# Performance work log

Hardware: AMD Instinct MI355X
Metric: run time of the kernel (lower is better)

## Reference

```python
import jax, jax.numpy as jnp
import numpy as np

K = 8
DIM = 64
NUM_BLOCKS = 12
BN_EPS = 1e-5
LRELU_SLOPE = 0.01  # torch nn.LeakyReLU default negative_slope


def knn_indices(xyz, k):
    # xyz: [b, 3, n] -> idx [b, n, k] of k nearest neighbors (self included)
    x = jnp.transpose(xyz, (0, 2, 1))  # [b, n, 3]
    sq = jnp.sum(x * x, axis=-1)  # [b, n]
    d2 = sq[:, :, None] - 2.0 * jnp.einsum('bnd,bmd->bnm', x, x) + sq[:, None, :]
    _, idx = jax.lax.top_k(-d2, k)  # k smallest distances
    return idx


def group_point(points, idx):
    # points [b, d, n], idx [b, n, k] -> grouped [b, d, k, n]
    g = jax.vmap(lambda p, i: p[:, i])(points, idx)  # [b, d, n, k]
    return jnp.transpose(g, (0, 1, 3, 2))


def setup_inputs() -> dict:
    key = jax.random.key(0)
    ks = jax.random.split(key, 6)
    b, n = 8, 4096
    xyz = jax.random.normal(ks[0], (b, 3, n), dtype=jnp.float32)
    points = jax.random.normal(ks[1], (b, DIM, n), dtype=jnp.float32)
    # per-block params (note: the module's second Conv2d per block is never used
    # in forward — layers[4*idx+2] is applied to both center and grouped points)
    conv_w = jax.random.normal(ks[2], (NUM_BLOCKS, DIM, DIM), dtype=jnp.float32) * (1.0 / np.sqrt(DIM))
    conv_b = jax.random.normal(ks[3], (NUM_BLOCKS, DIM), dtype=jnp.float32) * 0.01
    bn_gamma = 1.0 + 0.1 * jax.random.normal(ks[4], (NUM_BLOCKS, DIM), dtype=jnp.float32)
    bn_beta = 0.1 * jax.random.normal(ks[5], (NUM_BLOCKS, DIM), dtype=jnp.float32)
    return {"xyz": xyz, "points": points, "conv_w": conv_w, "conv_b": conv_b,
            "bn_gamma": bn_gamma, "bn_beta": bn_beta}


def reference(xyz, points, conv_w, conv_b, bn_gamma, bn_beta):
    idx = knn_indices(xyz, K)  # fixed graph, computed once in block 0

    def block(p, params):
        w, b, g, be = params  # [DIM,DIM], [DIM], [DIM], [DIM]
        shortcut = p
        # BatchNorm1d (training-mode batch stats over batch & point dims)
        mean = jnp.mean(p, axis=(0, 2), keepdims=True)
        var = jnp.var(p, axis=(0, 2), keepdims=True)
        h = (p - mean) * jax.lax.rsqrt(var + BN_EPS) * g[None, :, None] + be[None, :, None]
        # LeakyReLU
        h = jnp.where(h >= 0, h, LRELU_SLOPE * h)
        # gather neighbor features: [b, d, k, n]
        grouped = group_point(h, idx)
        # shared 1x1 conv on center and grouped points
        center = jnp.einsum('od,bdn->bon', w, h) + b[None, :, None]            # [b,d,n]
        gconv = jnp.einsum('od,bdkn->bokn', w, grouped) + b[None, :, None, None]  # [b,d,k,n]
        # mean over concat([center[:, :, None], gconv], axis=2) == (center + sum_k gconv) / (k+1)
        new_p = (center + jnp.sum(gconv, axis=2)) / (K + 1) + shortcut
        return new_p, None

    out, _ = jax.lax.scan(block, points, (conv_w, conv_b, bn_gamma, bn_beta))
    return out
```

## Files before the change

kernel.cpp:

```cpp
#include <hip/hip_runtime.h>
#include <hip/hip_bf16.h>

#define NB     8
#define NPTS   4096
#define DIMC   64
#define KNN_K  8
#define NBLK   12
#define NREP   8

__global__ void zero_stats_kernel(float* __restrict__ stats) {
    int i = threadIdx.x + blockIdx.x * 256;
    if (i < 13 * NREP * 128) stats[i] = 0.0f;
}

__global__ __launch_bounds__(256) void prep_kernel(
        const float* __restrict__ xyz, float4* __restrict__ pts4g) {
#pragma clang fp contract(off)
    int g = blockIdx.x * 256 + threadIdx.x;
    int b = g >> 12, j = g & 4095;
    const float* xb = xyz + (size_t)b * 3 * NPTS;
    float x = xb[j];
    float y = xb[NPTS + j];
    float z = xb[2 * NPTS + j];
    float sq = (x * x + y * y) + z * z;
    pts4g[g] = make_float4(x, y, z, sq);
}

__global__ __launch_bounds__(256) void cast_kernel(
        const float* __restrict__ pts,
        float* __restrict__ P0, float* __restrict__ stats0) {
    __shared__ __align__(16) float tr[64 * 65];
    __shared__ float slotA[4 * 64], slotB[4 * 64];
    int wg = blockIdx.x;
    int b = wg & 7;
    int n0 = (wg >> 3) << 6;
    int rep = (wg >> 3) & (NREP - 1);
    int tid = threadIdx.x;
    int lane6 = tid & 63;
    int grp = tid >> 6;

    #pragma unroll
    for (int k = 0; k < 16; ++k) {
        int d = grp + (k << 2);
        float v = pts[(((size_t)((b << 6) + d)) << 12) + n0 + lane6];
        tr[d * 65 + lane6] = v;
    }
    __syncthreads();
    int c = lane6;
    float s = 0.0f, s2 = 0.0f;
    #pragma unroll
    for (int k = 0; k < 16; ++k) {
        int p = grp + (k << 2);
        float v = tr[c * 65 + p];
        P0[((size_t)((b << 12) + n0 + p)) * 64 + c] = v;
        s += v; s2 += v * v;
    }
    slotA[grp * 64 + c] = s;
    slotB[grp * 64 + c] = s2;
    __syncthreads();
    if (tid < 64) {
        float t = slotA[tid] + slotA[64 + tid] + slotA[128 + tid] + slotA[192 + tid];
        atomicAdd(&stats0[rep * 128 + tid], t);
    } else if (tid < 128) {
        int cc = tid - 64;
        float t = slotB[cc] + slotB[64 + cc] + slotB[128 + cc] + slotB[192 + cc];
        atomicAdd(&stats0[rep * 128 + 64 + cc], t);
    }
}

__global__ __launch_bounds__(512) void knn_kernel(
        const float4* __restrict__ pts4g, int* __restrict__ idx) {
#pragma clang fp contract(off)
    __shared__ __align__(16) float4 cand[2048];
    __shared__ double stash[4 * 9 * 128];
    int wg = blockIdx.x;
    int b = wg >> 5;
    int q0 = (wg & 31) << 7;
    int tid = threadIdx.x;

    int lane  = tid & 63;
    int wave  = tid >> 6;
    int chunk = wave & 3;
    int qgrp  = wave >> 2;
    int q_l   = (qgrp << 6) | lane;

    const float4* cb = pts4g + ((size_t)b << 12);
    float4 qp = cb[q0 + q_l];

    double k0, k1, k2, k3, k4, k5, k6, k7;
    k0 = k1 = k2 = k3 = k4 = k5 = k6 = k7 = __builtin_inf();
    float bd7f = 3.4e38f;

    for (int half = 0; half < 2; ++half) {
        if (half) __syncthreads();
        #pragma unroll
        for (int k = 0; k < 4; ++k)
            cand[tid + (k << 9)] = cb[(half << 11) + tid + (k << 9)];
        __syncthreads();

        int jl0 = chunk << 9;
        int jg0 = (half << 11) | (chunk << 9);
        for (int jo = 0; jo < 512; jo += 8) {
            float d2v[8];
            #pragma unroll
            for (int u = 0; u < 8; ++u) {
                float4 p = cand[jl0 + jo + u];
                float dot = (qp.x * p.x + qp.y * p.y) + qp.z * p.z;
                d2v[u] = (qp.w - 2.0f * dot) + p.w;
            }
            #pragma unroll
            for (int u = 0; u < 8; ++u) {
                float d2 = d2v[u];
                if (d2 < bd7f) {
                    unsigned long long kb =
                        __double_as_longlong((double)d2) |
                        (unsigned long long)(jg0 + jo + u);
                    double key = __longlong_as_double(kb);
                    double n0 = fmin(k0, key);
                    double n1 = fmin(k1, fmax(k0, key));
                    double n2 = fmin(k2, fmax(k1, key));
                    double n3 = fmin(k3, fmax(k2, key));
                    double n4 = fmin(k4, fmax(k3, key));
                    double n5 = fmin(k5, fmax(k4, key));
                    double n6 = fmin(k6, fmax(k5, key));
                    double n7 = fmin(k7, fmax(k6, key));
                    k0 = n0; k1 = n1; k2 = n2; k3 = n3;
                    k4 = n4; k5 = n5; k6 = n6; k7 = n7;
                    bd7f = (float)k7;
                }
            }
        }
    }

    {
        double* S = &stash[(chunk * 9) * 128 + q_l];
        S[0 * 128] = k0; S[1 * 128] = k1; S[2 * 128] = k2; S[3 * 128] = k3;
        S[4 * 128] = k4; S[5 * 128] = k5; S[6 * 128] = k6; S[7 * 128] = k7;
        S[8 * 128] = __builtin_inf();
    }
    __syncthreads();

    if (tid < 128) {
        int h0 = 0, h1 = 0, h2 = 0, h3 = 0;
        int* op = idx + ((size_t)(b * NPTS + q0 + tid)) * 8;
        #pragma unroll
        for (int t = 0; t < 8; ++t) {
            double b0 = stash[(0 * 9 + h0) * 128 + tid];
            double b1 = stash[(1 * 9 + h1) * 128 + tid];
            double b2 = stash[(2 * 9 + h2) * 128 + tid];
            double b3 = stash[(3 * 9 + h3) * 128 + tid];
            double best = b0; int bc = 0;
            if (b1 < best) { best = b1; bc = 1; }
            if (b2 < best) { best = b2; bc = 2; }
            if (b3 < best) { best = b3; bc = 3; }
            h0 += (bc == 0); h1 += (bc == 1);
            h2 += (bc == 2); h3 += (bc == 3);
            op[t] = (int)(__double_as_longlong(best) & 0xFFFULL);
        }
    }
}

__global__ __launch_bounds__(256) void block_kernel(
        const float* __restrict__ Pin, float* __restrict__ Pout,
        const float* __restrict__ statsIn, float* __restrict__ statsOut,
        const float* __restrict__ Wp, const float* __restrict__ Bp,
        const float* __restrict__ Gp, const float* __restrict__ Betap,
        const int* __restrict__ gidx, float* __restrict__ dout, int last) {
    __shared__ __align__(16) float Wt[64 * 68];
    __shared__ __align__(16) float mt[64 * 68];
    __shared__ __align__(16) float selft[64 * 64];
    __shared__ __align__(16) int   idxl[64 * 8];
    __shared__ __align__(16) float scale_l[64], shift_l[64], bias_l[64];
    __shared__ float slot[4 * 128];

    int wg = blockIdx.x;
    int b = wg & 7;
    int n0 = (wg >> 3) << 6;
    int rep = (wg >> 3) & (NREP - 1);
    int tid = threadIdx.x;

    const float* Pb = Pin + (((size_t)b) << 18);

    if (tid < 128) {
        ((int4*)idxl)[tid] = ((const int4*)(gidx + ((size_t)(b * NPTS + n0)) * 8))[tid];
    }
    #pragma unroll
    for (int k = 0; k < 4; ++k) {
        int lin = tid + (k << 8);
        ((float4*)selft)[lin] = ((const float4*)&Pb[(size_t)n0 << 6])[lin];
    }
    #pragma unroll
    for (int k = 0; k < 16; ++k) {
        int lin = tid + (k << 8);
        int o = lin >> 6, d = lin & 63;
        Wt[d * 68 + o] = Wp[lin];
    }
    if (tid < 64) {
        int c = tid;
        float sum = 0.0f, sumsq = 0.0f;
        #pragma unroll
        for (int r = 0; r < NREP; ++r) {
            sum   += statsIn[r * 128 + c];
            sumsq += statsIn[r * 128 + 64 + c];
        }
        float mean = sum * (1.0f / 32768.0f);
        float var  = sumsq * (1.0f / 32768.0f) - mean * mean;
        float rs   = 1.0f / sqrtf(var + 1e-5f);
        float sc   = Gp[c] * rs;
        scale_l[c] = sc;
        shift_l[c] = Betap[c] - mean * sc;
        bias_l[c]  = Bp[c];
    }
    __syncthreads();

    {
        int cq = tid & 15;
        int pg = tid >> 4;
        int c4 = cq << 2;
        float4 sc4 = *(const float4*)&scale_l[c4];
        float4 sh4 = *(const float4*)&shift_l[c4];
        #pragma unroll
        for (int i = 0; i < 4; ++i) {
            int pt = (pg << 2) + i;
            int4 ja = *(const int4*)&idxl[pt * 8];
            int4 jb = *(const int4*)&idxl[pt * 8 + 4];
            float4 v[9];
            v[0] = *(const float4*)&selft[(pt << 6) + c4];
            v[1] = *(const float4*)&Pb[(((size_t)ja.x) << 6) + c4];
            v[2] = *(const float4*)&Pb[(((size_t)ja.y) << 6) + c4];
            v[3] = *(const float4*)&Pb[(((size_t)ja.z) << 6) + c4];
            v[4] = *(const float4*)&Pb[(((size_t)ja.w) << 6) + c4];
            v[5] = *(const float4*)&Pb[(((size_t)jb.x) << 6) + c4];
            v[6] = *(const float4*)&Pb[(((size_t)jb.y) << 6) + c4];
            v[7] = *(const float4*)&Pb[(((size_t)jb.z) << 6) + c4];
            v[8] = *(const float4*)&Pb[(((size_t)jb.w) << 6) + c4];
            float4 a = make_float4(0.f, 0.f, 0.f, 0.f);
            #pragma unroll
            for (int k = 0; k < 9; ++k) {
                float hx = v[k].x * sc4.x + sh4.x;
                float hy = v[k].y * sc4.y + sh4.y;
                float hz = v[k].z * sc4.z + sh4.z;
                float hw = v[k].w * sc4.w + sh4.w;
                a.x += fmaxf(hx, 0.01f * hx);
                a.y += fmaxf(hy, 0.01f * hy);
                a.z += fmaxf(hz, 0.01f * hz);
                a.w += fmaxf(hw, 0.01f * hw);
            }
            mt[(c4 + 0) * 68 + pt] = a.x * (1.0f / 9.0f);
            mt[(c4 + 1) * 68 + pt] = a.y * (1.0f / 9.0f);
            mt[(c4 + 2) * 68 + pt] = a.z * (1.0f / 9.0f);
            mt[(c4 + 3) * 68 + pt] = a.w * (1.0f / 9.0f);
        }
    }
    __syncthreads();

    int o0 = (tid & 15) << 2;
    int p0 = (tid >> 4) << 2;
    float4 acc[4];
    {
        float4 bias4 = *(const float4*)&bias_l[o0];
        acc[0] = bias4; acc[1] = bias4; acc[2] = bias4; acc[3] = bias4;
    }
    #pragma unroll
    for (int d = 0; d < 64; ++d) {
        float4 wv = *(const float4*)&Wt[d * 68 + o0];
        float4 a  = *(const float4*)&mt[d * 68 + p0];
        acc[0].x += wv.x * a.x; acc[0].y += wv.y * a.x; acc[0].z += wv.z * a.x; acc[0].w += wv.w * a.x;
        acc[1].x += wv.x * a.y; acc[1].y += wv.y * a.y; acc[1].z += wv.z * a.y; acc[1].w += wv.w * a.y;
        acc[2].x += wv.x * a.z; acc[2].y += wv.y * a.z; acc[2].z += wv.z * a.z; acc[2].w += wv.w * a.z;
        acc[3].x += wv.x * a.w; acc[3].y += wv.y * a.w; acc[3].z += wv.z * a.w; acc[3].w += wv.w * a.w;
    }

    #pragma unroll
    for (int j = 0; j < 4; ++j) {
        float4 r = *(const float4*)&selft[((p0 + j) << 6) + o0];
        acc[j].x += r.x; acc[j].y += r.y; acc[j].z += r.z; acc[j].w += r.w;
    }

    if (!last) {
        float* PbOut = Pout + ((((size_t)b) << 12) + n0) * 64;
        #pragma unroll
        for (int j = 0; j < 4; ++j)
            *(float4*)&PbOut[((size_t)(p0 + j)) * 64 + o0] = acc[j];

        float4 s, s2;
        s.x = acc[0].x + acc[1].x + acc[2].x + acc[3].x;
        s.y = acc[0].y + acc[1].y + acc[2].y + acc[3].y;
        s.z = acc[0].z + acc[1].z + acc[2].z + acc[3].z;
        s.w = acc[0].w + acc[1].w + acc[2].w + acc[3].w;
        s2.x = acc[0].x*acc[0].x + acc[1].x*acc[1].x + acc[2].x*acc[2].x + acc[3].x*acc[3].x;
        s2.y = acc[0].y*acc[0].y + acc[1].y*acc[1].y + acc[2].y*acc[2].y + acc[3].y*acc[3].y;
        s2.z = acc[0].z*acc[0].z + acc[1].z*acc[1].z + acc[2].z*acc[2].z + acc[3].z*acc[3].z;
        s2.w = acc[0].w*acc[0].w + acc[1].w*acc[1].w + acc[2].w*acc[2].w + acc[3].w*acc[3].w;
        #pragma unroll
        for (int m = 16; m <= 32; m <<= 1) {
            s.x += __shfl_xor(s.x, m, 64);  s.y += __shfl_xor(s.y, m, 64);
            s.z += __shfl_xor(s.z, m, 64);  s.w += __shfl_xor(s.w, m, 64);
            s2.x += __shfl_xor(s2.x, m, 64); s2.y += __shfl_xor(s2.y, m, 64);
            s2.z += __shfl_xor(s2.z, m, 64); s2.w += __shfl_xor(s2.w, m, 64);
        }
        if ((tid & 63) < 16) {
            int w = tid >> 6;
            slot[w * 128 + o0 + 0] = s.x;  slot[w * 128 + o0 + 1] = s.y;
            slot[w * 128 + o0 + 2] = s.z;  slot[w * 128 + o0 + 3] = s.w;
            slot[w * 128 + 64 + o0 + 0] = s2.x; slot[w * 128 + 64 + o0 + 1] = s2.y;
            slot[w * 128 + 64 + o0 + 2] = s2.z; slot[w * 128 + 64 + o0 + 3] = s2.w;
        }
        __syncthreads();
        if (tid < 128) {
            float t = slot[tid] + slot[128 + tid] + slot[256 + tid] + slot[384 + tid];
            atomicAdd(&statsOut[rep * 128 + tid], t);
        }
    } else {
        __syncthreads();
        float* stage = mt;
        #pragma unroll
        for (int j = 0; j < 4; ++j) {
            stage[(o0 + 0) * 64 + p0 + j] = acc[j].x;
            stage[(o0 + 1) * 64 + p0 + j] = acc[j].y;
            stage[(o0 + 2) * 64 + p0 + j] = acc[j].z;
            stage[(o0 + 3) * 64 + p0 + j] = acc[j].w;
        }
        __syncthreads();
        #pragma unroll
        for (int k = 0; k < 16; ++k) {
            int lin = tid + (k << 8);
            int o = lin >> 6, pt = lin & 63;
            dout[(((size_t)((b << 6) + o)) << 12) + n0 + pt] = stage[lin];
        }
    }
}

extern "C" void kernel_launch(void* const* d_in, const int* in_sizes, int n_in,
                              void* d_out, int out_size, void* d_ws, size_t ws_size,
                              hipStream_t stream) {
    const float* xyz    = (const float*)d_in[0];
    const float* pts    = (const float*)d_in[1];
    const float* conv_w = (const float*)d_in[2];
    const float* conv_b = (const float*)d_in[3];
    const float* gamma  = (const float*)d_in[4];
    const float* beta   = (const float*)d_in[5];
    float* out = (float*)d_out;

    char* ws = (char*)d_ws;
    float*  P0    = (float*)(ws);
    float*  P1    = (float*)(ws + (size_t)8 * 1024 * 1024);
    int*    idx   = (int*)  (ws + (size_t)16 * 1024 * 1024);
    float*  stats = (float*)(ws + (size_t)17 * 1024 * 1024);
    float4* pts4g = (float4*)(ws + (size_t)18 * 1024 * 1024);

    zero_stats_kernel<<<52, 256, 0, stream>>>(stats);
    prep_kernel<<<128, 256, 0, stream>>>(xyz, pts4g);
    cast_kernel<<<512, 256, 0, stream>>>(pts, P0, stats);
    knn_kernel<<<256, 512, 0, stream>>>(pts4g, idx);

    float* Pbuf[2] = {P0, P1};
    for (int t = 0; t < NBLK; ++t) {
        block_kernel<<<512, 256, 0, stream>>>(
            Pbuf[t & 1], Pbuf[(t + 1) & 1],
            stats + (size_t)t * NREP * 128, stats + (size_t)(t + 1) * NREP * 128,
            conv_w + (size_t)t * 4096, conv_b + (size_t)t * 64,
            gamma + (size_t)t * 64, beta + (size_t)t * 64,
            idx, out, (t == NBLK - 1) ? 1 : 0);
    }
}
```

Before: 326.7 us.

## Split kNN candidates across eight waves and widen block kernel to 512 threads

The kNN kernel now gives each workgroup 64 queries and splits the candidate scan into eight 256-point chunks, one per wave. It launches twice as many workgroups and merges eight partial top-8 lists instead of four. The residual block kernel moves to 512 threads, with each thread computing 2 points instead of 4, which raises thread-level parallelism at the cost of register reuse in the matmul. Stats zeroing is folded into the prep kernel to save one launch. Each kNN workgroup now loads all candidate points into shared memory, so there are twice as many shared-memory fills.

```diff
diff --git a/kernel.cpp b/kernel.cpp
--- a/kernel.cpp
+++ b/kernel.cpp
@@ -8,15 +8,12 @@
 #define NBLK   12
 #define NREP   8
 
-__global__ void zero_stats_kernel(float* __restrict__ stats) {
-    int i = threadIdx.x + blockIdx.x * 256;
-    if (i < 13 * NREP * 128) stats[i] = 0.0f;
-}
-
 __global__ __launch_bounds__(256) void prep_kernel(
-        const float* __restrict__ xyz, float4* __restrict__ pts4g) {
+        const float* __restrict__ xyz, float4* __restrict__ pts4g,
+        float* __restrict__ stats) {
 #pragma clang fp contract(off)
     int g = blockIdx.x * 256 + threadIdx.x;
+    if (g < 13 * NREP * 128) stats[g] = 0.0f;
     int b = g >> 12, j = g & 4095;
     const float* xb = xyz + (size_t)b * 3 * NPTS;
     float x = xb[j];
@@ -72,20 +69,17 @@
         const float4* __restrict__ pts4g, int* __restrict__ idx) {
 #pragma clang fp contract(off)
     __shared__ __align__(16) float4 cand[2048];
-    __shared__ double stash[4 * 9 * 128];
+    __shared__ double stash[8 * 9 * 64];
     int wg = blockIdx.x;
-    int b = wg >> 5;
-    int q0 = (wg & 31) << 7;
+    int b = wg >> 6;
+    int q0 = (wg & 63) << 6;
     int tid = threadIdx.x;
 
     int lane  = tid & 63;
-    int wave  = tid >> 6;
-    int chunk = wave & 3;
-    int qgrp  = wave >> 2;
-    int q_l   = (qgrp << 6) | lane;
+    int chunk = tid >> 6;
 
     const float4* cb = pts4g + ((size_t)b << 12);
-    float4 qp = cb[q0 + q_l];
+    float4 qp = cb[q0 + lane];
 
     double k0, k1, k2, k3, k4, k5, k6, k7;
     k0 = k1 = k2 = k3 = k4 = k5 = k6 = k7 = __builtin_inf();
@@ -98,9 +92,9 @@
             cand[tid + (k << 9)] = cb[(half << 11) + tid + (k << 9)];
         __syncthreads();
 
-        int jl0 = chunk << 9;
-        int jg0 = (half << 11) | (chunk << 9);
-        for (int jo = 0; jo < 512; jo += 8) {
+        int jl0 = chunk << 8;
+        int jg0 = (half << 11) | jl0;
+        for (int jo = 0; jo < 256; jo += 8) {
             float d2v[8];
             #pragma unroll
             for (int u = 0; u < 8; ++u) {
@@ -133,34 +127,42 @@
     }
 
     {
-        double* S = &stash[(chunk * 9) * 128 + q_l];
-        S[0 * 128] = k0; S[1 * 128] = k1; S[2 * 128] = k2; S[3 * 128] = k3;
-        S[4 * 128] = k4; S[5 * 128] = k5; S[6 * 128] = k6; S[7 * 128] = k7;
-        S[8 * 128] = __builtin_inf();
-    }
-    __syncthreads();
-
-    if (tid < 128) {
-        int h0 = 0, h1 = 0, h2 = 0, h3 = 0;
+        double* S = &stash[(chunk * 9) * 64 + lane];
+        S[0 * 64] = k0; S[1 * 64] = k1; S[2 * 64] = k2; S[3 * 64] = k3;
+        S[4 * 64] = k4; S[5 * 64] = k5; S[6 * 64] = k6; S[7 * 64] = k7;
+        S[8 * 64] = __builtin_inf();
+    }
+    __syncthreads();
+
+    if (tid < 64) {
+        int h0 = 0, h1 = 0, h2 = 0, h3 = 0, h4 = 0, h5 = 0, h6 = 0, h7 = 0;
         int* op = idx + ((size_t)(b * NPTS + q0 + tid)) * 8;
         #pragma unroll
         for (int t = 0; t < 8; ++t) {
-            double b0 = stash[(0 * 9 + h0) * 128 + tid];
-            double b1 = stash[(1 * 9 + h1) * 128 + tid];
-            double b2 = stash[(2 * 9 + h2) * 128 + tid];
-            double b3 = stash[(3 * 9 + h3) * 128 + tid];
-            double best = b0; int bc = 0;
-            if (b1 < best) { best = b1; bc = 1; }
-            if (b2 < best) { best = b2; bc = 2; }
-            if (b3 < best) { best = b3; bc = 3; }
-            h0 += (bc == 0); h1 += (bc == 1);
-            h2 += (bc == 2); h3 += (bc == 3);
+            double v0 = stash[(0 * 9 + h0) * 64 + tid];
+            double v1 = stash[(1 * 9 + h1) * 64 + tid];
+            double v2 = stash[(2 * 9 + h2) * 64 + tid];
+            double v3 = stash[(3 * 9 + h3) * 64 + tid];
+            double v4 = stash[(4 * 9 + h4) * 64 + tid];
+            double v5 = stash[(5 * 9 + h5) * 64 + tid];
+            double v6 = stash[(6 * 9 + h6) * 64 + tid];
+            double v7 = stash[(7 * 9 + h7) * 64 + tid];
+            double best = v0; int bc = 0;
+            if (v1 < best) { best = v1; bc = 1; }
+            if (v2 < best) { best = v2; bc = 2; }
+            if (v3 < best) { best = v3; bc = 3; }
+            if (v4 < best) { best = v4; bc = 4; }
+            if (v5 < best) { best = v5; bc = 5; }
+            if (v6 < best) { best = v6; bc = 6; }
+            if (v7 < best) { best = v7; bc = 7; }
+            h0 += (bc == 0); h1 += (bc == 1); h2 += (bc == 2); h3 += (bc == 3);
+            h4 += (bc == 4); h5 += (bc == 5); h6 += (bc == 6); h7 += (bc == 7);
             op[t] = (int)(__double_as_longlong(best) & 0xFFFULL);
         }
     }
 }
 
-__global__ __launch_bounds__(256) void block_kernel(
+__global__ __launch_bounds__(512) void block_kernel(
         const float* __restrict__ Pin, float* __restrict__ Pout,
         const float* __restrict__ statsIn, float* __restrict__ statsOut,
         const float* __restrict__ Wp, const float* __restrict__ Bp,
@@ -171,7 +173,7 @@
     __shared__ __align__(16) float selft[64 * 64];
     __shared__ __align__(16) int   idxl[64 * 8];
     __shared__ __align__(16) float scale_l[64], shift_l[64], bias_l[64];
-    __shared__ float slot[4 * 128];
+    __shared__ float slot[8 * 128];
 
     int wg = blockIdx.x;
     int b = wg & 7;
@@ -185,13 +187,13 @@
         ((int4*)idxl)[tid] = ((const int4*)(gidx + ((size_t)(b * NPTS + n0)) * 8))[tid];
     }
     #pragma unroll
-    for (int k = 0; k < 4; ++k) {
-        int lin = tid + (k << 8);
+    for (int k = 0; k < 2; ++k) {
+        int lin = tid + (k << 9);
         ((float4*)selft)[lin] = ((const float4*)&Pb[(size_t)n0 << 6])[lin];
     }
     #pragma unroll
-    for (int k = 0; k < 16; ++k) {
-        int lin = tid + (k << 8);
+    for (int k = 0; k < 8; ++k) {
+        int lin = tid + (k << 9);
         int o = lin >> 6, d = lin & 63;
         Wt[d * 68 + o] = Wp[lin];
     }
@@ -215,13 +217,13 @@
 
     {
         int cq = tid & 15;
-        int pg = tid >> 4;
+        int pp = tid >> 4;
         int c4 = cq << 2;
         float4 sc4 = *(const float4*)&scale_l[c4];
         float4 sh4 = *(const float4*)&shift_l[c4];
         #pragma unroll
-        for (int i = 0; i < 4; ++i) {
-            int pt = (pg << 2) + i;
+        for (int i = 0; i < 2; ++i) {
+            int pt = (pp << 1) + i;
             int4 ja = *(const int4*)&idxl[pt * 8];
             int4 jb = *(const int4*)&idxl[pt * 8 + 4];
             float4 v[9];
@@ -255,24 +257,22 @@
     __syncthreads();
 
     int o0 = (tid & 15) << 2;
-    int p0 = (tid >> 4) << 2;
-    float4 acc[4];
+    int p0 = (tid >> 4) << 1;
+    float4 acc[2];
     {
         float4 bias4 = *(const float4*)&bias_l[o0];
-        acc[0] = bias4; acc[1] = bias4; acc[2] = bias4; acc[3] = bias4;
+        acc[0] = bias4; acc[1] = bias4;
     }
     #pragma unroll
     for (int d = 0; d < 64; ++d) {
         float4 wv = *(const float4*)&Wt[d * 68 + o0];
-        float4 a  = *(const float4*)&mt[d * 68 + p0];
+        float2 a  = *(const float2*)&mt[d * 68 + p0];
         acc[0].x += wv.x * a.x; acc[0].y += wv.y * a.x; acc[0].z += wv.z * a.x; acc[0].w += wv.w * a.x;
         acc[1].x += wv.x * a.y; acc[1].y += wv.y * a.y; acc[1].z += wv.z * a.y; acc[1].w += wv.w * a.y;
-        acc[2].x += wv.x * a.z; acc[2].y += wv.y * a.z; acc[2].z += wv.z * a.z; acc[2].w += wv.w * a.z;
-        acc[3].x += wv.x * a.w; acc[3].y += wv.y * a.w; acc[3].z += wv.z * a.w; acc[3].w += wv.w * a.w;
-    }
-
-    #pragma unroll
-    for (int j = 0; j < 4; ++j) {
+    }
+
+    #pragma unroll
+    for (int j = 0; j < 2; ++j) {
         float4 r = *(const float4*)&selft[((p0 + j) << 6) + o0];
         acc[j].x += r.x; acc[j].y += r.y; acc[j].z += r.z; acc[j].w += r.w;
     }
@@ -280,18 +280,16 @@
     if (!last) {
         float* PbOut = Pout + ((((size_t)b) << 12) + n0) * 64;
         #pragma unroll
-        for (int j = 0; j < 4; ++j)
+        for (int j = 0; j < 2; ++j)
             *(float4*)&PbOut[((size_t)(p0 + j)) * 64 + o0] = acc[j];
 
         float4 s, s2;
-        s.x = acc[0].x + acc[1].x + acc[2].x + acc[3].x;
-        s.y = acc[0].y + acc[1].y + acc[2].y + acc[3].y;
-        s.z = acc[0].z + acc[1].z + acc[2].z + acc[3].z;
-        s.w = acc[0].w + acc[1].w + acc[2].w + acc[3].w;
-        s2.x = acc[0].x*acc[0].x + acc[1].x*acc[1].x + acc[2].x*acc[2].x + acc[3].x*acc[3].x;
-        s2.y = acc[0].y*acc[0].y + acc[1].y*acc[1].y + acc[2].y*acc[2].y + acc[3].y*acc[3].y;
-        s2.z = acc[0].z*acc[0].z + acc[1].z*acc[1].z + acc[2].z*acc[2].z + acc[3].z*acc[3].z;
-        s2.w = acc[0].w*acc[0].w + acc[1].w*acc[1].w + acc[2].w*acc[2].w + acc[3].w*acc[3].w;
+        s.x = acc[0].x + acc[1].x;  s.y = acc[0].y + acc[1].y;
+        s.z = acc[0].z + acc[1].z;  s.w = acc[0].w + acc[1].w;
+        s2.x = acc[0].x*acc[0].x + acc[1].x*acc[1].x;
+        s2.y = acc[0].y*acc[0].y + acc[1].y*acc[1].y;
+        s2.z = acc[0].z*acc[0].z + acc[1].z*acc[1].z;
+        s2.w = acc[0].w*acc[0].w + acc[1].w*acc[1].w;
         #pragma unroll
         for (int m = 16; m <= 32; m <<= 1) {
             s.x += __shfl_xor(s.x, m, 64);  s.y += __shfl_xor(s.y, m, 64);
@@ -308,14 +306,16 @@
         }
         __syncthreads();
         if (tid < 128) {
-            float t = slot[tid] + slot[128 + tid] + slot[256 + tid] + slot[384 + tid];
+            float t = 0.0f;
+            #pragma unroll
+            for (int w = 0; w < 8; ++w) t += slot[w * 128 + tid];
             atomicAdd(&statsOut[rep * 128 + tid], t);
         }
     } else {
         __syncthreads();
         float* stage = mt;
         #pragma unroll
-        for (int j = 0; j < 4; ++j) {
+        for (int j = 0; j < 2; ++j) {
             stage[(o0 + 0) * 64 + p0 + j] = acc[j].x;
             stage[(o0 + 1) * 64 + p0 + j] = acc[j].y;
             stage[(o0 + 2) * 64 + p0 + j] = acc[j].z;
@@ -323,8 +323,8 @@
         }
         __syncthreads();
         #pragma unroll
-        for (int k = 0; k < 16; ++k) {
-            int lin = tid + (k << 8);
+        for (int k = 0; k < 8; ++k) {
+            int lin = tid + (k << 9);
             int o = lin >> 6, pt = lin & 63;
             dout[(((size_t)((b << 6) + o)) << 12) + n0 + pt] = stage[lin];
         }
@@ -349,14 +349,13 @@
     float*  stats = (float*)(ws + (size_t)17 * 1024 * 1024);
     float4* pts4g = (float4*)(ws + (size_t)18 * 1024 * 1024);
 
-    zero_stats_kernel<<<52, 256, 0, stream>>>(stats);
-    prep_kernel<<<128, 256, 0, stream>>>(xyz, pts4g);
+    prep_kernel<<<128, 256, 0, stream>>>(xyz, pts4g, stats);
     cast_kernel<<<512, 256, 0, stream>>>(pts, P0, stats);
-    knn_kernel<<<256, 512, 0, stream>>>(pts4g, idx);
+    knn_kernel<<<512, 512, 0, stream>>>(pts4g, idx);
 
     float* Pbuf[2] = {P0, P1};
     for (int t = 0; t < NBLK; ++t) {
-        block_kernel<<<512, 256, 0, stream>>>(
+        block_kernel<<<512, 512, 0, stream>>>(
             Pbuf[t & 1], Pbuf[(t + 1) & 1],
             stats + (size_t)t * NREP * 128, stats + (size_t)(t + 1) * NREP * 128,
             conv_w + (size_t)t * 4096, conv_b + (size_t)t * 64,
```

Result: slower. 336.0 us (+2.8%).
